# Kernel optimization log

Measured on AMD Instinct MI355X. Metric: run time of the kernel, lower is better.

Reference implementation:

```python
import jax, jax.numpy as jnp
import numpy as np

B = 1024
P = 8
D = 2048
NUM_IDS = 64
MARGIN = 0.3
EPS = 1e-12


def setup_inputs() -> dict:
    key = jax.random.key(0)
    k1, k2, k3 = jax.random.split(key, 3)
    feats = jax.random.normal(k1, (B, P * D), dtype=jnp.float32)
    labels = jax.random.randint(k2, (B,), 0, NUM_IDS, dtype=jnp.int64)
    subs = jax.random.randint(k3, (B,), 0, 2, dtype=jnp.int64)
    return {"feats": feats, "labels": labels, "subs": subs}


def reference(feats, labels, subs):
    b = feats.shape[0]
    f = feats.reshape(b, -1, D)  # [B, P, D]
    dt = f.dtype

    # Per-sample class centers via a single segment-mean pass
    # (equivalent to the original per-sample boolean-mask mean loop).
    seg_sum = jax.ops.segment_sum(f, labels, num_segments=NUM_IDS)  # [NUM_IDS, P, D]
    counts = jax.ops.segment_sum(jnp.ones((b,), dt), labels, num_segments=NUM_IDS)
    centers_by_id = seg_sum / jnp.maximum(counts, 1.0)[:, None, None]
    centers = centers_by_id[labels]  # [B, P, D]

    # dist_ap[i] = sum_p ||f[i,p] - center[i,p]||
    d_ap = jnp.sqrt(jnp.clip(jnp.sum((f - centers) ** 2, axis=-1), EPS, None)).sum(-1)  # [B]
    dist_ap = d_ap[:, None] + d_ap[None, :]  # [B, B]

    # pairwise_distance: dist_aa[i,j] = sum_p ||f[i,p] - f[j,p]||, via gemm trick
    sq = jnp.sum(f * f, axis=-1)  # [B, P]
    inner = jnp.einsum('ipd,jpd->ijp', f, f)  # [B, B, P]
    d2 = sq[:, None, :] + sq[None, :, :] - 2.0 * inner
    dist_aa = jnp.sqrt(jnp.clip(d2, EPS, None)).sum(-1)  # [B, B]

    # masked margin loss over negative (different-label) pairs
    mask = labels[:, None] != labels[None, :]  # [B, B] bool
    vals = jnp.clip(dist_ap - dist_aa + MARGIN, 0.0, None)
    maskf = mask.astype(dt)
    loss = jnp.sum(vals * maskf) / jnp.sum(maskf)
    return loss
```

## Files before the change

kernel.cpp:

```cpp
#include <hip/hip_runtime.h>
#include <hip/hip_bf16.h>

#define B_ 1024
#define P_ 8
#define D_ 2048
#define FD_ (P_ * D_)
#define NID 64
#define MARGIN_ 0.3f
#define EPS_ 1e-12f
#define NJOBS 576

typedef unsigned short u16;
typedef float float4_t __attribute__((ext_vector_type(4)));

#define AS1 __attribute__((address_space(1)))
#define AS3 __attribute__((address_space(3)))

__device__ __forceinline__ float bf2f(u16 v) {
    unsigned x = (unsigned)v << 16;
    float f;
    __builtin_memcpy(&f, &x, 4);
    return f;
}

static const size_t OFF_COUNTS = 0;
static const size_t OFF_OFFS   = 256;
static const size_t OFF_PERM   = 512;
static const size_t OFF_NEG    = 4608;
static const size_t OFF_DONE   = 4616;
static const size_t OFF_POS    = 8176;
static const size_t OFF_S      = 8192;
static const size_t OFF_SQ     = 40960;
static const size_t OFF_DAP    = 73728;
static const size_t OFF_FB     = 131072;
static const size_t OFF_PD     = OFF_FB + (size_t)B_ * FD_;

__global__ void k_prep(const float* __restrict__ feats, const int* __restrict__ labels,
                       unsigned char* __restrict__ fb, float* __restrict__ sq,
                       float* countsf, int* offs, int* perm, float* negcnt,
                       float* S, float* possum, int* done) {
    int tid = threadIdx.x;
    if (blockIdx.x < B_) {
        int i = blockIdx.x;
        int w = tid >> 6, lane = tid & 63;
        const float* frow = feats + (size_t)i * FD_;
        unsigned char* brow = fb + (size_t)i * FD_;
#pragma unroll
        for (int pp = 0; pp < 2; pp++) {
            int p = w * 2 + pp;
            int off = p * D_;
            float s2 = 0.f;
#pragma unroll
            for (int ch = 0; ch < 8; ch++) {
                int d = off + ch * 256 + lane * 4;
                float4 f = *(const float4*)(frow + d);
                int pk = __builtin_amdgcn_cvt_pk_fp8_f32(f.x, f.y, 0, false);
                pk = __builtin_amdgcn_cvt_pk_fp8_f32(f.z, f.w, pk, true);
                *(unsigned int*)(brow + d) = (unsigned int)pk;
                s2 += f.x * f.x + f.y * f.y + f.z * f.z + f.w * f.w;
            }
            for (int o = 32; o; o >>= 1) s2 += __shfl_down(s2, o, 64);
            if (lane == 0) sq[i * P_ + p] = s2;
        }
        return;
    }
    __shared__ int h[NID], o[NID], cur[NID];
    if (tid < NID) h[tid] = 0;
    __syncthreads();
    for (int i = tid; i < B_; i += 256) atomicAdd(&h[labels[i]], 1);
    __syncthreads();
    if (tid == 0) {
        int acc = 0;
        long long ss = 0;
        for (int c = 0; c < NID; c++) {
            o[c] = acc;
            acc += h[c];
            ss += (long long)h[c] * h[c];
        }
        *negcnt = (float)((long long)B_ * B_ - ss);
        *possum = 0.f;
        done[0] = 0;
    }
    __syncthreads();
    if (tid < NID) {
        countsf[tid] = (float)h[tid];
        offs[tid] = o[tid];
        cur[tid] = o[tid];
    }
    __syncthreads();
    for (int i = tid; i < B_; i += 256) {
        int pos = atomicAdd(&cur[labels[i]], 1);
        perm[pos] = i;
    }
    for (int i = tid; i < B_ * P_; i += 256) S[i] = 0.f;
}

__global__ __launch_bounds__(256, 3) void k_pairs(const unsigned char* __restrict__ fb,
                                                  const float* __restrict__ sq,
                                                  const int* __restrict__ labels,
                                                  float* __restrict__ S,
                                                  u16* __restrict__ pd) {
    int t = blockIdx.x >> 3;
    const int p = blockIdx.x & 7;
    int ti = 0;
    while (t >= 16 - 2 * ti) { t -= 16 - 2 * ti; ti++; }
    const int ju = 2 * ti + t;
    const int i0 = ti * 128, j0 = ju * 64;
    const bool offdiag = (ju >= 2 * ti + 2);

    __shared__ __align__(16) unsigned char smem[49152];
    __shared__ float sqAs[128], sqBs[64];
    __shared__ int labA[128], labB[64];
    const int tid = threadIdx.x;
    const int lane = tid & 63, wid = tid >> 6;
    const int s = wid & 1, h = wid >> 1;
    if (tid < 128) {
        sqAs[tid] = sq[(i0 + tid) * 8 + p];
        labA[tid] = labels[i0 + tid];
    } else if (tid < 192) {
        int u = tid - 128;
        sqBs[u] = sq[(j0 + u) * 8 + p];
        labB[u] = labels[j0 + u];
    }

    const int wi = s * 64;
    const int lhi = lane >> 4, llo = lane & 15;
    const int sl = llo & 7;
    const int lr = lane >> 3;
    const int lc = (lane & 7) ^ lr;

    unsigned char* const As = smem + h * 16384;
    unsigned char* const Bs = smem + 32768 + h * 8192;

    const size_t colbase = (size_t)p * D_ + (size_t)h * 1024 + (size_t)lc * 16;
    const unsigned char* gA[8];
    unsigned char* lA[8];
    const unsigned char* gB[4];
    unsigned char* lB[4];
#pragma unroll
    for (int inst = 0; inst < 8; inst++) {
        int r0 = s * 64 + inst * 8;
        gA[inst] = fb + (size_t)(i0 + r0 + lr) * FD_ + colbase;
        lA[inst] = As + r0 * 128;
    }
#pragma unroll
    for (int inst = 0; inst < 4; inst++) {
        int r0 = s * 32 + inst * 8;
        gB[inst] = fb + (size_t)(j0 + r0 + lr) * FD_ + colbase;
        lB[inst] = Bs + r0 * 128;
    }

    float4_t acc[4][4];
#pragma unroll
    for (int a = 0; a < 4; a++)
#pragma unroll
        for (int b = 0; b < 4; b++) acc[a][b] = (float4_t){0.f, 0.f, 0.f, 0.f};

    for (int kb = 0; kb < 8; kb++) {
        const int koff = kb * 128;
        __syncthreads();
#pragma unroll
        for (int inst = 0; inst < 8; inst++)
            __builtin_amdgcn_global_load_lds((const AS1 void*)(gA[inst] + koff),
                                             (AS3 void*)lA[inst], 16, 0, 0);
#pragma unroll
        for (int inst = 0; inst < 4; inst++)
            __builtin_amdgcn_global_load_lds((const AS1 void*)(gB[inst] + koff),
                                             (AS3 void*)lB[inst], 16, 0, 0);
        __syncthreads();
#pragma unroll
        for (int ks = 0; ks < 4; ks++) {
            const int pcb = ((2 * ks + (lhi >> 1)) ^ sl) * 16 + (lhi & 1) * 8;
            long af[4], bf[4];
#pragma unroll
            for (int a = 0; a < 4; a++) {
                af[a] = *(const long*)(As + (wi + a * 16 + llo) * 128 + pcb);
                bf[a] = *(const long*)(Bs + (a * 16 + llo) * 128 + pcb);
            }
#pragma unroll
            for (int a = 0; a < 4; a++)
#pragma unroll
                for (int b = 0; b < 4; b++)
                    acc[a][b] = __builtin_amdgcn_mfma_f32_16x16x32_fp8_fp8(
                        af[a], bf[b], acc[a][b], 0, 0, 0);
        }
    }
    __syncthreads();
    float* ep = (float*)smem;
    if (h == 1) {
#pragma unroll
        for (int a = 0; a < 4; a++)
#pragma unroll
            for (int b = 0; b < 4; b++)
                *(float4_t*)&ep[(((s * 4 + a) * 4 + b) * 64 + lane) * 4] = acc[a][b];
    }
    __syncthreads();
    if (h == 0) {
        u16* outp = pd + (size_t)p * B_ * B_;
        float rs[4][4];
        float cs[4];
#pragma unroll
        for (int a = 0; a < 4; a++)
#pragma unroll
            for (int r = 0; r < 4; r++) rs[a][r] = 0.f;
#pragma unroll
        for (int b = 0; b < 4; b++) cs[b] = 0.f;
#pragma unroll
        for (int a = 0; a < 4; a++) {
            int la0 = labA[wi + a * 16 + lhi * 4 + 0];
            int la1 = labA[wi + a * 16 + lhi * 4 + 1];
            int la2 = labA[wi + a * 16 + lhi * 4 + 2];
            int la3 = labA[wi + a * 16 + lhi * 4 + 3];
#pragma unroll
            for (int b = 0; b < 4; b++) {
                float4_t o = *(const float4_t*)&ep[(((s * 4 + a) * 4 + b) * 64 + lane) * 4];
                int jl = b * 16 + llo;
                int lb = labB[jl];
#pragma unroll
                for (int r = 0; r < 4; r++) {
                    int il = wi + a * 16 + lhi * 4 + r;
                    float tt = acc[a][b][r] + o[r];
                    float d2 = sqAs[il] + sqBs[jl] - 2.0f * tt;
                    u16 bv = __bfloat16_as_ushort(__float2bfloat16(sqrtf(fmaxf(d2, EPS_))));
                    outp[(size_t)(i0 + il) * B_ + (j0 + jl)] = bv;
                    if (offdiag) outp[(size_t)(j0 + jl) * B_ + (i0 + il)] = bv;
                    int la = (r == 0) ? la0 : (r == 1) ? la1 : (r == 2) ? la2 : la3;
                    if (lb == la) {
                        rs[a][r] += tt;
                        if (offdiag) cs[b] += tt;
                    }
                }
            }
        }
#pragma unroll
        for (int a = 0; a < 4; a++)
#pragma unroll
            for (int r = 0; r < 4; r++) {
                float v = rs[a][r];
                v += __shfl_xor(v, 1, 64);
                v += __shfl_xor(v, 2, 64);
                v += __shfl_xor(v, 4, 64);
                v += __shfl_xor(v, 8, 64);
                if (llo == 0)
                    atomicAdd(&S[(size_t)(i0 + wi + a * 16 + lhi * 4 + r) * 8 + p], v);
            }
        if (offdiag) {
#pragma unroll
            for (int b = 0; b < 4; b++) {
                float v = cs[b];
                v += __shfl_xor(v, 16, 64);
                v += __shfl_xor(v, 32, 64);
                if (lhi == 0)
                    atomicAdd(&S[(size_t)(j0 + b * 16 + llo) * 8 + p], v);
            }
        }
    }
}

__global__ void k_dap(const float* __restrict__ S, const float* __restrict__ sq,
                      const float* __restrict__ countsf, const int* __restrict__ offs,
                      const int* __restrict__ perm, float* __restrict__ dap) {
    int c = blockIdx.x;
    int tid = threadIdx.x;
    int cnt = (int)countsf[c];
    int off = offs[c];
    __shared__ float T[8];
    if (tid < 8) {
        float t = 0.f;
        for (int m = 0; m < cnt; m++) t += S[(size_t)perm[off + m] * 8 + tid];
        T[tid] = t;
    }
    __syncthreads();
    float n = fmaxf((float)cnt, 1.f);
    float inv = 1.f / n, inv2 = inv * inv;
    for (int m = tid; m < cnt; m += 64) {
        int i = perm[off + m];
        float d = 0.f;
#pragma unroll
        for (int p = 0; p < 8; p++) {
            float d2 = sq[i * 8 + p] - 2.f * inv * S[(size_t)i * 8 + p] + inv2 * T[p];
            d += sqrtf(fmaxf(d2, EPS_));
        }
        dap[i] = d;
    }
}

__global__ void k_lossred(const u16* __restrict__ pd, const float* __restrict__ dap,
                          const int* __restrict__ labels, float* possum,
                          const float* __restrict__ negcnt, int* __restrict__ done,
                          float* __restrict__ out) {
    int i = blockIdx.x;
    int tid = threadIdx.x;
    float di = dap[i];
    int li = labels[i];
    int j0 = tid * 4;
    float d0 = 0.f, d1 = 0.f, d2 = 0.f, d3 = 0.f;
#pragma unroll
    for (int p = 0; p < P_; p++) {
        ushort4 v = *(const ushort4*)&pd[(size_t)p * B_ * B_ + (size_t)i * B_ + j0];
        d0 += bf2f(v.x);
        d1 += bf2f(v.y);
        d2 += bf2f(v.z);
        d3 += bf2f(v.w);
    }
    int4 lj = *(const int4*)&labels[j0];
    float4 dj = *(const float4*)&dap[j0];
    float lsum = 0.f;
    if (lj.x != li) lsum += fmaxf(di + dj.x - d0 + MARGIN_, 0.f);
    if (lj.y != li) lsum += fmaxf(di + dj.y - d1 + MARGIN_, 0.f);
    if (lj.z != li) lsum += fmaxf(di + dj.z - d2 + MARGIN_, 0.f);
    if (lj.w != li) lsum += fmaxf(di + dj.w - d3 + MARGIN_, 0.f);
    for (int o = 32; o; o >>= 1) lsum += __shfl_down(lsum, o, 64);
    __shared__ float red[4];
    int wid = tid >> 6, lane = tid & 63;
    if (lane == 0) red[wid] = lsum;
    __syncthreads();
    if (tid == 0) {
        atomicAdd(possum, red[0] + red[1] + red[2] + red[3]);
        __threadfence();
        int v = atomicAdd(done, 1);
        if (v == B_ - 1) {
            float ps = atomicAdd(possum, 0.f);
            out[0] = ps / negcnt[0];
        }
    }
}

extern "C" void kernel_launch(void* const* d_in, const int* in_sizes, int n_in,
                              void* d_out, int out_size, void* d_ws, size_t ws_size,
                              hipStream_t stream) {
    const float* feats = (const float*)d_in[0];
    const int* labels  = (const int*)d_in[1];
    float* out = (float*)d_out;

    char* w = (char*)d_ws;
    float* countsf = (float*)(w + OFF_COUNTS);
    int* offs      = (int*)(w + OFF_OFFS);
    int* perm      = (int*)(w + OFF_PERM);
    float* negcnt  = (float*)(w + OFF_NEG);
    int* done      = (int*)(w + OFF_DONE);
    float* possum  = (float*)(w + OFF_POS);
    float* S       = (float*)(w + OFF_S);
    float* sq      = (float*)(w + OFF_SQ);
    float* dap     = (float*)(w + OFF_DAP);
    unsigned char* fb = (unsigned char*)(w + OFF_FB);
    u16* pd        = (u16*)(w + OFF_PD);

    k_prep<<<B_ + 1, 256, 0, stream>>>(feats, labels, fb, sq, countsf, offs, perm,
                                       negcnt, S, possum, done);
    k_pairs<<<NJOBS, 256, 0, stream>>>(fb, sq, labels, S, pd);
    k_dap<<<NID, 64, 0, stream>>>(S, sq, countsf, offs, perm, dap);
    k_lossred<<<B_, 256, 0, stream>>>(pd, dap, labels, possum, negcnt, done, out);
}
```

Before: 167.8 us.

## Switch pair kernel to 64x64 tiles with 2x2 wave split, drop split-K reduction

The pairwise-distance kernel now uses 64x64 upper-triangular tiles (136 per part) instead of 128x64 tiles, and the four waves form a 2x2 grid over the output instead of splitting K in halves. This removes the LDS round trip and extra barrier that combined the split-K partial accumulators, shrinks shared memory to 16 KB, and raises the occupancy hint from 3 to 4. In exchange each tile reads more of the operand data per output, there are more blocks and more atomics, and each wave runs twice as many K iterations with fewer MFMAs per LDS load.

```diff
diff --git a/kernel.cpp b/kernel.cpp
--- a/kernel.cpp
+++ b/kernel.cpp
@@ -8,7 +8,7 @@
 #define NID 64
 #define MARGIN_ 0.3f
 #define EPS_ 1e-12f
-#define NJOBS 576
+#define NJOBS (136 * 8)
 
 typedef unsigned short u16;
 typedef float float4_t __attribute__((ext_vector_type(4)));
@@ -95,7 +95,7 @@
     for (int i = tid; i < B_ * P_; i += 256) S[i] = 0.f;
 }
 
-__global__ __launch_bounds__(256, 3) void k_pairs(const unsigned char* __restrict__ fb,
+__global__ __launch_bounds__(256, 4) void k_pairs(const unsigned char* __restrict__ fb,
                                                   const float* __restrict__ sq,
                                                   const int* __restrict__ labels,
                                                   float* __restrict__ S,
@@ -103,156 +103,138 @@
     int t = blockIdx.x >> 3;
     const int p = blockIdx.x & 7;
     int ti = 0;
-    while (t >= 16 - 2 * ti) { t -= 16 - 2 * ti; ti++; }
-    const int ju = 2 * ti + t;
-    const int i0 = ti * 128, j0 = ju * 64;
-    const bool offdiag = (ju >= 2 * ti + 2);
-
-    __shared__ __align__(16) unsigned char smem[49152];
-    __shared__ float sqAs[128], sqBs[64];
-    __shared__ int labA[128], labB[64];
+    while (t >= 16 - ti) { t -= 16 - ti; ti++; }
+    const int tj = ti + t;
+    const int i0 = ti * 64, j0 = tj * 64;
+    const bool offdiag = (tj > ti);
+
+    __shared__ __align__(16) unsigned char smem[16384];
+    __shared__ float sqAs[64], sqBs[64];
+    __shared__ int labA[64], labB[64];
     const int tid = threadIdx.x;
-    const int lane = tid & 63, wid = tid >> 6;
-    const int s = wid & 1, h = wid >> 1;
-    if (tid < 128) {
+    const int lane = tid & 63, w = tid >> 6;
+    const int wr = w >> 1, wc = w & 1;
+    if (tid < 64) {
         sqAs[tid] = sq[(i0 + tid) * 8 + p];
         labA[tid] = labels[i0 + tid];
-    } else if (tid < 192) {
-        int u = tid - 128;
+    } else if (tid < 128) {
+        int u = tid - 64;
         sqBs[u] = sq[(j0 + u) * 8 + p];
         labB[u] = labels[j0 + u];
     }
 
-    const int wi = s * 64;
     const int lhi = lane >> 4, llo = lane & 15;
     const int sl = llo & 7;
     const int lr = lane >> 3;
     const int lc = (lane & 7) ^ lr;
 
-    unsigned char* const As = smem + h * 16384;
-    unsigned char* const Bs = smem + 32768 + h * 8192;
-
-    const size_t colbase = (size_t)p * D_ + (size_t)h * 1024 + (size_t)lc * 16;
-    const unsigned char* gA[8];
-    unsigned char* lA[8];
-    const unsigned char* gB[4];
-    unsigned char* lB[4];
-#pragma unroll
-    for (int inst = 0; inst < 8; inst++) {
-        int r0 = s * 64 + inst * 8;
+    unsigned char* const As = smem;
+    unsigned char* const Bs = smem + 8192;
+
+    const size_t colbase = (size_t)p * D_ + (size_t)lc * 16;
+    const unsigned char* gA[2];
+    const unsigned char* gB[2];
+    unsigned char* lA[2];
+    unsigned char* lB[2];
+#pragma unroll
+    for (int inst = 0; inst < 2; inst++) {
+        int r0 = w * 16 + inst * 8;
         gA[inst] = fb + (size_t)(i0 + r0 + lr) * FD_ + colbase;
+        gB[inst] = fb + (size_t)(j0 + r0 + lr) * FD_ + colbase;
         lA[inst] = As + r0 * 128;
-    }
-#pragma unroll
-    for (int inst = 0; inst < 4; inst++) {
-        int r0 = s * 32 + inst * 8;
-        gB[inst] = fb + (size_t)(j0 + r0 + lr) * FD_ + colbase;
         lB[inst] = Bs + r0 * 128;
     }
 
-    float4_t acc[4][4];
-#pragma unroll
-    for (int a = 0; a < 4; a++)
-#pragma unroll
-        for (int b = 0; b < 4; b++) acc[a][b] = (float4_t){0.f, 0.f, 0.f, 0.f};
-
-    for (int kb = 0; kb < 8; kb++) {
+    float4_t acc[2][2];
+#pragma unroll
+    for (int a = 0; a < 2; a++)
+#pragma unroll
+        for (int b = 0; b < 2; b++) acc[a][b] = (float4_t){0.f, 0.f, 0.f, 0.f};
+
+    for (int kb = 0; kb < 16; kb++) {
         const int koff = kb * 128;
         __syncthreads();
 #pragma unroll
-        for (int inst = 0; inst < 8; inst++)
+        for (int inst = 0; inst < 2; inst++) {
             __builtin_amdgcn_global_load_lds((const AS1 void*)(gA[inst] + koff),
                                              (AS3 void*)lA[inst], 16, 0, 0);
-#pragma unroll
-        for (int inst = 0; inst < 4; inst++)
             __builtin_amdgcn_global_load_lds((const AS1 void*)(gB[inst] + koff),
                                              (AS3 void*)lB[inst], 16, 0, 0);
+        }
         __syncthreads();
 #pragma unroll
         for (int ks = 0; ks < 4; ks++) {
             const int pcb = ((2 * ks + (lhi >> 1)) ^ sl) * 16 + (lhi & 1) * 8;
-            long af[4], bf[4];
-#pragma unroll
-            for (int a = 0; a < 4; a++) {
-                af[a] = *(const long*)(As + (wi + a * 16 + llo) * 128 + pcb);
-                bf[a] = *(const long*)(Bs + (a * 16 + llo) * 128 + pcb);
+            long af[2], bf[2];
+#pragma unroll
+            for (int a = 0; a < 2; a++) {
+                af[a] = *(const long*)(As + (wr * 32 + a * 16 + llo) * 128 + pcb);
+                bf[a] = *(const long*)(Bs + (wc * 32 + a * 16 + llo) * 128 + pcb);
             }
 #pragma unroll
-            for (int a = 0; a < 4; a++)
-#pragma unroll
-                for (int b = 0; b < 4; b++)
+            for (int a = 0; a < 2; a++)
+#pragma unroll
+                for (int b = 0; b < 2; b++)
                     acc[a][b] = __builtin_amdgcn_mfma_f32_16x16x32_fp8_fp8(
                         af[a], bf[b], acc[a][b], 0, 0, 0);
         }
     }
-    __syncthreads();
-    float* ep = (float*)smem;
-    if (h == 1) {
-#pragma unroll
-        for (int a = 0; a < 4; a++)
-#pragma unroll
-            for (int b = 0; b < 4; b++)
-                *(float4_t*)&ep[(((s * 4 + a) * 4 + b) * 64 + lane) * 4] = acc[a][b];
-    }
-    __syncthreads();
-    if (h == 0) {
-        u16* outp = pd + (size_t)p * B_ * B_;
-        float rs[4][4];
-        float cs[4];
-#pragma unroll
-        for (int a = 0; a < 4; a++)
-#pragma unroll
-            for (int r = 0; r < 4; r++) rs[a][r] = 0.f;
-#pragma unroll
-        for (int b = 0; b < 4; b++) cs[b] = 0.f;
-#pragma unroll
-        for (int a = 0; a < 4; a++) {
-            int la0 = labA[wi + a * 16 + lhi * 4 + 0];
-            int la1 = labA[wi + a * 16 + lhi * 4 + 1];
-            int la2 = labA[wi + a * 16 + lhi * 4 + 2];
-            int la3 = labA[wi + a * 16 + lhi * 4 + 3];
-#pragma unroll
-            for (int b = 0; b < 4; b++) {
-                float4_t o = *(const float4_t*)&ep[(((s * 4 + a) * 4 + b) * 64 + lane) * 4];
-                int jl = b * 16 + llo;
-                int lb = labB[jl];
-#pragma unroll
-                for (int r = 0; r < 4; r++) {
-                    int il = wi + a * 16 + lhi * 4 + r;
-                    float tt = acc[a][b][r] + o[r];
-                    float d2 = sqAs[il] + sqBs[jl] - 2.0f * tt;
-                    u16 bv = __bfloat16_as_ushort(__float2bfloat16(sqrtf(fmaxf(d2, EPS_))));
-                    outp[(size_t)(i0 + il) * B_ + (j0 + jl)] = bv;
-                    if (offdiag) outp[(size_t)(j0 + jl) * B_ + (i0 + il)] = bv;
-                    int la = (r == 0) ? la0 : (r == 1) ? la1 : (r == 2) ? la2 : la3;
-                    if (lb == la) {
-                        rs[a][r] += tt;
-                        if (offdiag) cs[b] += tt;
-                    }
+
+    u16* outp = pd + (size_t)p * B_ * B_;
+    float rs[2][4];
+    float cs[2];
+#pragma unroll
+    for (int a = 0; a < 2; a++)
+#pragma unroll
+        for (int r = 0; r < 4; r++) rs[a][r] = 0.f;
+#pragma unroll
+    for (int b = 0; b < 2; b++) cs[b] = 0.f;
+#pragma unroll
+    for (int a = 0; a < 2; a++) {
+        int la0 = labA[wr * 32 + a * 16 + lhi * 4 + 0];
+        int la1 = labA[wr * 32 + a * 16 + lhi * 4 + 1];
+        int la2 = labA[wr * 32 + a * 16 + lhi * 4 + 2];
+        int la3 = labA[wr * 32 + a * 16 + lhi * 4 + 3];
+#pragma unroll
+        for (int b = 0; b < 2; b++) {
+            int jl = wc * 32 + b * 16 + llo;
+            int lb = labB[jl];
+#pragma unroll
+            for (int r = 0; r < 4; r++) {
+                int il = wr * 32 + a * 16 + lhi * 4 + r;
+                float tt = acc[a][b][r];
+                float d2 = sqAs[il] + sqBs[jl] - 2.0f * tt;
+                u16 bv = __bfloat16_as_ushort(__float2bfloat16(sqrtf(fmaxf(d2, EPS_))));
+                outp[(size_t)(i0 + il) * B_ + (j0 + jl)] = bv;
+                if (offdiag) outp[(size_t)(j0 + jl) * B_ + (i0 + il)] = bv;
+                int la = (r == 0) ? la0 : (r == 1) ? la1 : (r == 2) ? la2 : la3;
+                if (lb == la) {
+                    rs[a][r] += tt;
+                    if (offdiag) cs[b] += tt;
                 }
             }
         }
-#pragma unroll
-        for (int a = 0; a < 4; a++)
-#pragma unroll
-            for (int r = 0; r < 4; r++) {
-                float v = rs[a][r];
-                v += __shfl_xor(v, 1, 64);
-                v += __shfl_xor(v, 2, 64);
-                v += __shfl_xor(v, 4, 64);
-                v += __shfl_xor(v, 8, 64);
-                if (llo == 0)
-                    atomicAdd(&S[(size_t)(i0 + wi + a * 16 + lhi * 4 + r) * 8 + p], v);
-            }
-        if (offdiag) {
-#pragma unroll
-            for (int b = 0; b < 4; b++) {
-                float v = cs[b];
-                v += __shfl_xor(v, 16, 64);
-                v += __shfl_xor(v, 32, 64);
-                if (lhi == 0)
-                    atomicAdd(&S[(size_t)(j0 + b * 16 + llo) * 8 + p], v);
-            }
+    }
+#pragma unroll
+    for (int a = 0; a < 2; a++)
+#pragma unroll
+        for (int r = 0; r < 4; r++) {
+            float v = rs[a][r];
+            v += __shfl_xor(v, 1, 64);
+            v += __shfl_xor(v, 2, 64);
+            v += __shfl_xor(v, 4, 64);
+            v += __shfl_xor(v, 8, 64);
+            if (llo == 0)
+                atomicAdd(&S[(size_t)(i0 + wr * 32 + a * 16 + lhi * 4 + r) * 8 + p], v);
+        }
+    if (offdiag) {
+#pragma unroll
+        for (int b = 0; b < 2; b++) {
+            float v = cs[b];
+            v += __shfl_xor(v, 16, 64);
+            v += __shfl_xor(v, 32, 64);
+            if (lhi == 0)
+                atomicAdd(&S[(size_t)(j0 + wc * 32 + b * 16 + llo) * 8 + p], v);
         }
     }
 }
```

After: 177.6 us. 5.8% more time.
